# Optimization experiments

Measured on AMD Instinct MI355X. Metric: run time of the kernel, lower is better.

## Reference

```python
import jax, jax.numpy as jnp
import numpy as np

B, T, HOR = 4096, 128, 24
EH, DH, A = 64, 64, 32


def setup_inputs() -> dict:
    key = jax.random.key(0)
    ks = jax.random.split(key, 21)
    g = lambda k, shape, s=0.1: (jax.random.normal(k, shape, jnp.float32) * s)
    return {
        "x": jax.random.normal(ks[0], (B, T, 1), jnp.float32),
        # encoder GRUCell (input_size=1)
        "W_ih_e": g(ks[1], (3 * EH, 1)), "W_hh_e": g(ks[2], (3 * EH, EH)),
        "b_ih_e": g(ks[3], (3 * EH,)), "b_hh_e": g(ks[4], (3 * EH,)),
        # encoder input attention
        "W_e": g(ks[5], (A, EH)), "U_e": g(ks[6], (1, A)),
        "b_e": jnp.zeros((1, A), jnp.float32), "v_e": g(ks[7], (A,)),
        # decoder init
        "W_init": g(ks[8], (DH, EH)), "b_init": g(ks[9], (DH,)),
        # decoder GRUCell (input_size=1)
        "W_ih_d": g(ks[10], (3 * DH, 1)), "W_hh_d": g(ks[11], (3 * DH, DH)),
        "b_ih_d": g(ks[12], (3 * DH,)), "b_hh_d": g(ks[13], (3 * DH,)),
        # temporal attention
        "W_d": g(ks[14], (A, DH)), "U_d": g(ks[15], (A, EH)), "v_d": g(ks[16], (A,)),
        # output head
        "W_out": g(ks[17], (1, DH + EH)), "b_out": g(ks[18], (1,)),
        "y0": jnp.zeros((1,), jnp.float32),
    }


def _gru_cell(x, h, W_ih, W_hh, b_ih, b_hh):
    # PyTorch GRUCell semantics
    gi = x @ W_ih.T + b_ih  # (B, 3H)
    gh = h @ W_hh.T + b_hh
    ir, iz, inn = jnp.split(gi, 3, axis=1)
    hr, hz, hn = jnp.split(gh, 3, axis=1)
    r = jax.nn.sigmoid(ir + hr)
    z = jax.nn.sigmoid(iz + hz)
    n = jnp.tanh(inn + r * hn)
    return (1.0 - z) * n + z * h


def reference(x, W_ih_e, W_hh_e, b_ih_e, b_hh_e, W_e, U_e, b_e, v_e,
              W_init, b_init, W_ih_d, W_hh_d, b_ih_d, b_hh_d,
              W_d, U_d, v_d, W_out, b_out, y0):
    bsz = x.shape[0]

    def enc_step(h, x_t):  # x_t: (B, 1)
        h_proj = h @ W_e.T  # (B, A)
        attn = jnp.tanh(h_proj[:, None, :] + x_t[:, :, None] * U_e[None] + b_e[None])  # (B,1,A)
        scores = jnp.sum(attn * v_e, axis=2)  # (B, 1)
        alpha = jax.nn.softmax(scores, axis=1)
        h_new = _gru_cell(alpha * x_t, h, W_ih_e, W_hh_e, b_ih_e, b_hh_e)
        return h_new, h_new

    h0 = jnp.zeros((bsz, EH), x.dtype)
    h_T, Hs = jax.lax.scan(enc_step, h0, jnp.swapaxes(x, 0, 1))  # Hs: (T,B,EH)
    H = jnp.swapaxes(Hs, 0, 1)  # (B, T, EH)

    d0 = h_T @ W_init.T + b_init  # (B, DH)
    H_proj = jnp.einsum('bte,ae->bta', H, U_d)  # hoisted: constant across decoder steps
    dec_in0 = jnp.broadcast_to(y0[None, :], (bsz, 1))

    def dec_step(carry, _):
        d, dec_in = carry
        d = _gru_cell(dec_in, d, W_ih_d, W_hh_d, b_ih_d, b_hh_d)
        d_proj = d @ W_d.T  # (B, A)
        attn = jnp.tanh(d_proj[:, None, :] + H_proj)  # (B, T, A)
        beta = jax.nn.softmax(jnp.sum(attn * v_d, axis=2), axis=1)  # (B, T)
        ctx = jnp.einsum('bt,bte->be', beta, H)  # (B, EH)
        out = jnp.concatenate([d, ctx], axis=1) @ W_out.T + b_out  # (B, 1)
        return (d, out), out[:, 0]

    (_, _), outs = jax.lax.scan(dec_step, (d0, dec_in0), None, length=HOR)
    return outs.T  # (B, horizon)
```

## Files before the change

### kernel.cpp

```cpp
#include <hip/hip_runtime.h>
#include <math.h>

#define BATCH 4096
#define T 128
#define HOR 24

#define LOG2E 1.44269504088896f
#define C2    2.88539008177793f

typedef _Float16 half2_t __attribute__((ext_vector_type(2)));
typedef _Float16 half8   __attribute__((ext_vector_type(8)));
typedef float f2  __attribute__((ext_vector_type(2)));
typedef float f4v __attribute__((ext_vector_type(4)));

__device__ __forceinline__ float fexp2(float x){ return __builtin_amdgcn_exp2f(x); }
__device__ __forceinline__ float frcp(float x){ return __builtin_amdgcn_rcpf(x); }
__device__ __forceinline__ float fsig(float x){ return frcp(1.0f + fexp2(-LOG2E*x)); }
__device__ __forceinline__ float ftanh(float x){ return fmaf(-2.0f, frcp(1.0f + fexp2(C2*x)), 1.0f); }
__device__ __forceinline__ half2_t bch(unsigned u){ return __builtin_bit_cast(half2_t,u); }
__device__ __forceinline__ unsigned pk2(float a,float b){ return __builtin_bit_cast(unsigned, __builtin_amdgcn_cvt_pkrtz(a,b)); }
__device__ __forceinline__ unsigned pk2rne(float a,float b){
  half2_t h; h.x = (_Float16)a; h.y = (_Float16)b;
  return __builtin_bit_cast(unsigned, h);
}
__device__ __forceinline__ float fdot2f(half2_t a, half2_t b, float c){
#if __has_builtin(__builtin_amdgcn_fdot2)
  return __builtin_amdgcn_fdot2(a,b,c,false);
#else
  return fmaf((float)a.x,(float)b.x, fmaf((float)a.y,(float)b.y,c));
#endif
}
__device__ __forceinline__ f2 pkfma(f2 a, f2 b, f2 c){ return __builtin_elementwise_fma(a,b,c); }

template <int CTRL, int RMASK>
__device__ __forceinline__ float dpp_add(float v) {
  int s = __builtin_amdgcn_update_dpp(0, __builtin_bit_cast(int, v), CTRL, RMASK, 0xf, true);
  return v + __builtin_bit_cast(float, s);
}
__device__ __forceinline__ float wavesum_dpp(float v) {
  v = dpp_add<0x111, 0xf>(v);
  v = dpp_add<0x112, 0xf>(v);
  v = dpp_add<0x114, 0xf>(v);
  v = dpp_add<0x118, 0xf>(v);
  v = dpp_add<0x142, 0xa>(v);
  v = dpp_add<0x143, 0xc>(v);
  return v;
}
__device__ __forceinline__ float rdl63(float v){
  return __builtin_bit_cast(float, __builtin_amdgcn_readlane(__builtin_bit_cast(int, v), 63));
}

#define WG_BARRIER_LDS() do {                                   \
    asm volatile("s_waitcnt lgkmcnt(0)" ::: "memory");          \
    __builtin_amdgcn_s_barrier();                               \
  } while (0)

__device__ __forceinline__ void gru_mv(const _Float16* hrow,
    const unsigned* wr_r, const unsigned* wr_z, const unsigned* wr_n,
    float& ar0, float& ar1, float& az0, float& az1, float& an0, float& an1)
{
  const uint4* hq = (const uint4*)hrow;
  #pragma unroll
  for (int q = 0; q < 8; ++q) {
    uint4 hv = hq[q];
    ar0 = fdot2f(bch(hv.x), bch(wr_r[4*q+0]), ar0);
    az0 = fdot2f(bch(hv.x), bch(wr_z[4*q+0]), az0);
    an0 = fdot2f(bch(hv.x), bch(wr_n[4*q+0]), an0);
    ar1 = fdot2f(bch(hv.y), bch(wr_r[4*q+1]), ar1);
    az1 = fdot2f(bch(hv.y), bch(wr_z[4*q+1]), az1);
    an1 = fdot2f(bch(hv.y), bch(wr_n[4*q+1]), an1);
    ar0 = fdot2f(bch(hv.z), bch(wr_r[4*q+2]), ar0);
    az0 = fdot2f(bch(hv.z), bch(wr_z[4*q+2]), az0);
    an0 = fdot2f(bch(hv.z), bch(wr_n[4*q+2]), an0);
    ar1 = fdot2f(bch(hv.w), bch(wr_r[4*q+3]), ar1);
    az1 = fdot2f(bch(hv.w), bch(wr_z[4*q+3]), az1);
    an1 = fdot2f(bch(hv.w), bch(wr_n[4*q+3]), an1);
  }
}

__device__ __forceinline__ float proj_dot(const _Float16* base, const unsigned* udr)
{
  float acc = 0.f;
  const uint4* hb = (const uint4*)base;
  #pragma unroll
  for (int q = 0; q < 4; ++q) {
    uint4 hv = hb[q];
    acc = fdot2f(bch(hv.x), bch(udr[4*q+0]), acc);
    acc = fdot2f(bch(hv.y), bch(udr[4*q+1]), acc);
    acc = fdot2f(bch(hv.z), bch(udr[4*q+2]), acc);
    acc = fdot2f(bch(hv.w), bch(udr[4*q+3]), acc);
  }
  return acc;
}

__device__ __forceinline__ half8 cvt8(f4v a, f4v b){
  half8 h;
  h[0]=(_Float16)a.x; h[1]=(_Float16)a.y; h[2]=(_Float16)a.z; h[3]=(_Float16)a.w;
  h[4]=(_Float16)b.x; h[5]=(_Float16)b.y; h[6]=(_Float16)b.z; h[7]=(_Float16)b.w;
  return h;
}

__global__ __launch_bounds__(256, 1)
void darnn_enc(const float* __restrict__ x,
               const float* __restrict__ W_ih_e, const float* __restrict__ W_hh_e,
               const float* __restrict__ b_ih_e, const float* __restrict__ b_hh_e,
               const float* __restrict__ U_d, const float* __restrict__ W_out,
               unsigned* __restrict__ hpG, float* __restrict__ hTG)
{
  const int tid = threadIdx.x;
  const int w = tid >> 6;
  const int l = tid & 63;
  const int c = l & 15;
  const int q = l >> 4;
  const int e0 = blockIdx.x * 16;
  const int m0 = 16*w + 4*q;

  __shared__ __align__(16) _Float16 He[2][16*72];
  __shared__ __align__(16) unsigned xw[16*65];
  __shared__ __align__(16) unsigned ehC[2][16*273];

  for (int idx = tid; idx < 16*64; idx += 256) {
    int e = idx >> 6, j = idx & 63;
    f2 g = ((const f2*)(x + (size_t)(e0+e)*T))[j];
    xw[e*65 + j] = pk2(g.x, g.y);
  }
  for (int idx = tid; idx < 576; idx += 256) ((unsigned*)He[0])[idx] = 0;

  half8 Ar[2], Az[2], An[2];
  #pragma unroll
  for (int kap = 0; kap < 2; ++kap) {
    const f4v* pr = (const f4v*)(W_hh_e + (size_t)(16*w + c)*64       + 32*kap + 8*q);
    const f4v* pz = (const f4v*)(W_hh_e + (size_t)(64 + 16*w + c)*64  + 32*kap + 8*q);
    const f4v* pn = (const f4v*)(W_hh_e + (size_t)(128 + 16*w + c)*64 + 32*kap + 8*q);
    Ar[kap] = cvt8(pr[0], pr[1]);
    Az[kap] = cvt8(pz[0], pz[1]);
    An[kap] = cvt8(pn[0], pn[1]);
  }
  half8 AX[2] = {{0,0,0,0,0,0,0,0},{0,0,0,0,0,0,0,0}};
  if (w < 2) {
    #pragma unroll
    for (int kap = 0; kap < 2; ++kap) {
      const f4v* p = (const f4v*)(U_d + (size_t)(16*w + c)*64 + 32*kap + 8*q);
      AX[kap] = cvt8(p[0] * C2, p[1] * C2);
    }
  } else if (w == 2 && c == 0) {
    #pragma unroll
    for (int kap = 0; kap < 2; ++kap) {
      const f4v* p = (const f4v*)(W_out + 64 + 32*kap + 8*q);
      AX[kap] = cvt8(p[0], p[1]);
    }
  }
  f4v wih0 = *(const f4v*)(W_ih_e + m0);
  f4v wih1 = *(const f4v*)(W_ih_e + 64 + m0);
  f4v wih2 = *(const f4v*)(W_ih_e + 128 + m0);
  f4v bb0  = *(const f4v*)(b_ih_e + m0)      + *(const f4v*)(b_hh_e + m0);
  f4v bb1  = *(const f4v*)(b_ih_e + 64 + m0) + *(const f4v*)(b_hh_e + 64 + m0);
  f4v bi2  = *(const f4v*)(b_ih_e + 128 + m0);
  f4v bh2  = *(const f4v*)(b_hh_e + 128 + m0);
  f4v hreg = {0,0,0,0};
  const f4v z4 = {0,0,0,0};

  __syncthreads();

  #pragma unroll 1
  for (int t = 0; t < T; ++t) {
    if ((t & 15) == 1 && t > 16) {
      int cidx = (t - 17) >> 4;
      const unsigned* sbuf = ehC[cidx & 1];
      int t0 = cidx << 4;
      #pragma unroll
      for (int it = 0; it < 17; ++it) {
        int idx = tid + it*256;
        int e = idx / 272;
        int o = idx - e*272;
        hpG[(size_t)(e0+e)*2176 + t0*17 + o] = sbuf[e*273 + o];
      }
    }
    const _Float16* Hc = He[t & 1];
    half8 B0 = __builtin_bit_cast(half8, *(const uint4*)(Hc + c*72 + 8*q));
    half8 B1 = __builtin_bit_cast(half8, *(const uint4*)(Hc + c*72 + 32 + 8*q));
    if (t > 0) {
      unsigned* eb = ehC[((t-1) >> 4) & 1] + c*273 + ((t-1) & 15)*17;
      if (w < 2) {
        f4v cu = __builtin_amdgcn_mfma_f32_16x16x32_f16(AX[0], B0, z4, 0,0,0);
        cu     = __builtin_amdgcn_mfma_f32_16x16x32_f16(AX[1], B1, cu, 0,0,0);
        float x0 = fexp2(fminf(cu[0], 15.5f));
        float x1 = fexp2(fminf(cu[1], 15.5f));
        float x2 = fexp2(fminf(cu[2], 15.5f));
        float x3 = fexp2(fminf(cu[3], 15.5f));
        eb[8*w + 2*q]   = pk2rne(x0, x1);
        eb[8*w + 2*q+1] = pk2rne(x2, x3);
      } else if (w == 2) {
        f4v cw = __builtin_amdgcn_mfma_f32_16x16x32_f16(AX[0], B0, z4, 0,0,0);
        cw     = __builtin_amdgcn_mfma_f32_16x16x32_f16(AX[1], B1, cw, 0,0,0);
        if (q == 0) ((float*)eb)[16] = cw[0];
      }
    }
    f4v gr = __builtin_amdgcn_mfma_f32_16x16x32_f16(Ar[0], B0, z4, 0,0,0);
    gr     = __builtin_amdgcn_mfma_f32_16x16x32_f16(Ar[1], B1, gr, 0,0,0);
    f4v gz = __builtin_amdgcn_mfma_f32_16x16x32_f16(Az[0], B0, z4, 0,0,0);
    gz     = __builtin_amdgcn_mfma_f32_16x16x32_f16(Az[1], B1, gz, 0,0,0);
    f4v gn = __builtin_amdgcn_mfma_f32_16x16x32_f16(An[0], B0, z4, 0,0,0);
    gn     = __builtin_amdgcn_mfma_f32_16x16x32_f16(An[1], B1, gn, 0,0,0);
    float xc = (float)((const _Float16*)xw)[c*130 + t];
    f4v hn;
    #pragma unroll
    for (int i = 0; i < 4; ++i) {
      float r  = fsig(fmaf(xc, wih0[i], bb0[i]) + gr[i]);
      float zf = fsig(fmaf(xc, wih1[i], bb1[i]) + gz[i]);
      float n  = ftanh(fmaf(xc, wih2[i], bi2[i]) + r*(gn[i] + bh2[i]));
      float h  = fmaf(zf, hreg[i] - n, n);
      hreg[i] = h;
      hn[i] = h;
    }
    uint2 wv; wv.x = pk2(hn[0], hn[1]); wv.y = pk2(hn[2], hn[3]);
    *(uint2*)(He[(t+1)&1] + c*72 + m0) = wv;
    WG_BARRIER_LDS();
  }
  {
    const _Float16* Hc = He[0];
    half8 B0 = __builtin_bit_cast(half8, *(const uint4*)(Hc + c*72 + 8*q));
    half8 B1 = __builtin_bit_cast(half8, *(const uint4*)(Hc + c*72 + 32 + 8*q));
    unsigned* eb = ehC[1] + c*273 + 15*17;
    if (w < 2) {
      f4v cu = __builtin_amdgcn_mfma_f32_16x16x32_f16(AX[0], B0, z4, 0,0,0);
      cu     = __builtin_amdgcn_mfma_f32_16x16x32_f16(AX[1], B1, cu, 0,0,0);
      float x0 = fexp2(fminf(cu[0], 15.5f));
      float x1 = fexp2(fminf(cu[1], 15.5f));
      float x2 = fexp2(fminf(cu[2], 15.5f));
      float x3 = fexp2(fminf(cu[3], 15.5f));
      eb[8*w + 2*q]   = pk2rne(x0, x1);
      eb[8*w + 2*q+1] = pk2rne(x2, x3);
    } else if (w == 2) {
      f4v cw = __builtin_amdgcn_mfma_f32_16x16x32_f16(AX[0], B0, z4, 0,0,0);
      cw     = __builtin_amdgcn_mfma_f32_16x16x32_f16(AX[1], B1, cw, 0,0,0);
      if (q == 0) ((float*)eb)[16] = cw[0];
    }
  }
  WG_BARRIER_LDS();
  {
    const unsigned* sbuf = ehC[1];
    #pragma unroll
    for (int it = 0; it < 17; ++it) {
      int idx = tid + it*256;
      int e = idx / 272;
      int o = idx - e*272;
      hpG[(size_t)(e0+e)*2176 + 112*17 + o] = sbuf[e*273 + o];
    }
  }
  #pragma unroll
  for (int i = 0; i < 4; ++i)
    hTG[(size_t)(e0 + c)*64 + m0 + i] = hreg[i];
}

__global__ __launch_bounds__(128, 2)
void darnn_dec(const float* __restrict__ W_init, const float* __restrict__ b_init,
               const float* __restrict__ W_ih_d, const float* __restrict__ W_hh_d,
               const float* __restrict__ b_ih_d, const float* __restrict__ b_hh_d,
               const float* __restrict__ W_d, const float* __restrict__ v_d,
               const float* __restrict__ W_out, const float* __restrict__ b_out,
               const float* __restrict__ y0,
               const unsigned* __restrict__ hpG, const float* __restrict__ hTG,
               float* __restrict__ out)
{
  const int tid = threadIdx.x;
  const int wid = tid >> 6;
  const int l   = tid & 63;
  const int bA  = 4*blockIdx.x + 2*wid;
  const int bB  = bA + 1;
  const int a    = l & 31;
  const int half = l >> 5;

  __shared__ __align__(16) unsigned char smem[36928];
  unsigned char* wbp = smem + wid*18464;
  unsigned* hpA   = (unsigned*)wbp;
  unsigned* hpB   = (unsigned*)(wbp + 8704);
  _Float16* ringA = (_Float16*)(wbp + 17408);
  _Float16* ringB = (_Float16*)(wbp + 17536);
  float*    dpA   = (float*)(wbp + 17664);
  float*    dpB   = (float*)(wbp + 17792);
  float*    hTA   = (float*)(wbp + 17920);
  float*    hTB   = (float*)(wbp + 18176);

  {
    const uint4* sA = (const uint4*)(hpG + (size_t)bA * 2176);
    const uint4* sB = (const uint4*)(hpG + (size_t)bB * 2176);
    #pragma unroll
    for (int it = 0; it < 8; ++it) {
      ((uint4*)hpA)[it*64 + l] = sA[it*64 + l];
      ((uint4*)hpB)[it*64 + l] = sB[it*64 + l];
    }
    const unsigned* rA = hpG + (size_t)bA*2176 + 2048;
    const unsigned* rB = hpG + (size_t)bB*2176 + 2048;
    hpA[2048 + l] = rA[l];      hpA[2112 + l] = rA[64 + l];
    hpB[2048 + l] = rB[l];      hpB[2112 + l] = rB[64 + l];
  }
  hTA[l] = hTG[(size_t)bA*64 + l];
  hTB[l] = hTG[(size_t)bB*64 + l];

  unsigned wr_r[32], wr_z[32], wr_n[32];
  {
    const f4v* wp = (const f4v*)W_hh_d;
    #pragma unroll
    for (int k = 0; k < 16; ++k) {
      f4v vr = wp[l*16 + k];
      f4v vz = wp[(64 + l)*16 + k];
      f4v vn = wp[(128 + l)*16 + k];
      wr_r[2*k] = pk2(vr.x, vr.y); wr_r[2*k+1] = pk2(vr.z, vr.w);
      wr_z[2*k] = pk2(vz.x, vz.y); wr_z[2*k+1] = pk2(vz.z, vz.w);
      wr_n[2*k] = pk2(vn.x, vn.y); wr_n[2*k+1] = pk2(vn.z, vn.w);
    }
  }
  float wih0 = W_ih_d[l], wih1 = W_ih_d[64+l], wih2 = W_ih_d[128+l];
  float bb0  = b_ih_d[l] + b_hh_d[l];
  float bb1  = b_ih_d[64+l] + b_hh_d[64+l];
  float bih2 = b_ih_d[128+l], bhh2 = b_hh_d[128+l];
  unsigned udr[16];
  {
    const f2* up = (const f2*)(W_d + a*64 + half*32);
    #pragma unroll
    for (int k = 0; k < 16; ++k) { f2 f = up[k]; udr[k] = pk2(f.x, f.y); }
  }
  float dprevA, dprevB;
  {
    const f4v* wi = (const f4v*)(W_init + l*64);
    const f4v* ga = (const f4v*)hTA;
    const f4v* gb = (const f4v*)hTB;
    f2 aa0={0,0}, aa1={0,0}, ba0={0,0}, ba1={0,0};
    #pragma unroll
    for (int k = 0; k < 16; ++k) {
      f4v wv = wi[k];
      f4v va = ga[k], vb = gb[k];
      aa0 = pkfma(wv.xy, va.xy, aa0);
      aa1 = pkfma(wv.zw, va.zw, aa1);
      ba0 = pkfma(wv.xy, vb.xy, ba0);
      ba1 = pkfma(wv.zw, vb.zw, ba1);
    }
    float bi = b_init[l];
    dprevA = bi + (aa0.x + aa0.y) + (aa1.x + aa1.y);
    dprevB = bi + (ba0.x + ba0.y) + (ba1.x + ba1.y);
  }
  float wout1 = W_out[l];
  float hw0A = __builtin_bit_cast(float, hpA[l*17 + 16]);
  float hw1A = __builtin_bit_cast(float, hpA[(64 + l)*17 + 16]);
  float hw0B = __builtin_bit_cast(float, hpB[l*17 + 16]);
  float hw1B = __builtin_bit_cast(float, hpB[(64 + l)*17 + 16]);
  float oprevA = y0[0], oprevB = y0[0];
  float bo = b_out[0];
  float c1;
  {
    float sv = v_d[a];
    sv += __shfl_xor(sv, 16); sv += __shfl_xor(sv, 8);
    sv += __shfl_xor(sv, 4);  sv += __shfl_xor(sv, 2); sv += __shfl_xor(sv, 1);
    c1 = LOG2E * sv;
  }
  ringA[l] = (_Float16)dprevA;
  ringB[l] = (_Float16)dprevB;

  const unsigned* hprA0 = hpA + l*17;
  const unsigned* hprA1 = hpA + (64 + l)*17;
  const unsigned* hprB0 = hpB + l*17;
  const unsigned* hprB1 = hpB + (64 + l)*17;

  #pragma unroll 1
  for (int s = 0; s < HOR; ++s) {
    float ar0A=0,ar1A=0,az0A=0,az1A=0,an0A=0,an1A=0;
    float ar0B=0,ar1B=0,az0B=0,az1B=0,an0B=0,an1B=0;
    gru_mv(ringA, wr_r, wr_z, wr_n, ar0A,ar1A,az0A,az1A,an0A,an1A);
    gru_mv(ringB, wr_r, wr_z, wr_n, ar0B,ar1B,az0B,az1B,an0B,an1B);
    float rA = fsig(fmaf(oprevA, wih0, bb0) + ar0A + ar1A);
    float zA = fsig(fmaf(oprevA, wih1, bb1) + az0A + az1A);
    float nA = ftanh(fmaf(oprevA, wih2, bih2) + rA * (an0A + an1A + bhh2));
    float dnewA = fmaf(zA, dprevA - nA, nA);
    float rB = fsig(fmaf(oprevB, wih0, bb0) + ar0B + ar1B);
    float zB = fsig(fmaf(oprevB, wih1, bb1) + az0B + az1B);
    float nB = ftanh(fmaf(oprevB, wih2, bih2) + rB * (an0B + an1B + bhh2));
    float dnewB = fmaf(zB, dprevB - nB, nB);
    dprevA = dnewA; dprevB = dnewB;
    ringA[l] = (_Float16)dnewA;
    ringB[l] = (_Float16)dnewB;
    {
      float accA = proj_dot(ringA + half*32, udr);
      float accB = proj_dot(ringB + half*32, udr);
      accA += __shfl_xor(accA, 32);
      accB += __shfl_xor(accB, 32);
      if (l < 32) {
        dpA[l] = fexp2(C2 * accA);
        dpB[l] = fexp2(C2 * accB);
      }
    }
    float rs0A = 0.f, rs1A = 0.f, rs0B = 0.f, rs1B = 0.f;
    #pragma unroll
    for (int j2 = 0; j2 < 8; ++j2) {
      f4v edA = *(const f4v*)&dpA[4*j2];
      f4v edB = *(const f4v*)&dpB[4*j2];
      half2_t haA0 = bch(hprA0[2*j2]), hbA0 = bch(hprA0[2*j2+1]);
      half2_t haA1 = bch(hprA1[2*j2]), hbA1 = bch(hprA1[2*j2+1]);
      half2_t haB0 = bch(hprB0[2*j2]), hbB0 = bch(hprB0[2*j2+1]);
      half2_t haB1 = bch(hprB1[2*j2]), hbB1 = bch(hprB1[2*j2+1]);
      float v0 = v_d[4*j2], v1 = v_d[4*j2+1], v2 = v_d[4*j2+2], v3 = v_d[4*j2+3];
      rs0A = fmaf(v0, frcp(fmaf(edA.x, (float)haA0.x, 1.0f)), rs0A);
      rs0B = fmaf(v0, frcp(fmaf(edB.x, (float)haB0.x, 1.0f)), rs0B);
      rs0A = fmaf(v1, frcp(fmaf(edA.y, (float)haA0.y, 1.0f)), rs0A);
      rs0B = fmaf(v1, frcp(fmaf(edB.y, (float)haB0.y, 1.0f)), rs0B);
      rs0A = fmaf(v2, frcp(fmaf(edA.z, (float)hbA0.x, 1.0f)), rs0A);
      rs0B = fmaf(v2, frcp(fmaf(edB.z, (float)hbB0.x, 1.0f)), rs0B);
      rs0A = fmaf(v3, frcp(fmaf(edA.w, (float)hbA0.y, 1.0f)), rs0A);
      rs0B = fmaf(v3, frcp(fmaf(edB.w, (float)hbB0.y, 1.0f)), rs0B);
      rs1A = fmaf(v0, frcp(fmaf(edA.x, (float)haA1.x, 1.0f)), rs1A);
      rs1B = fmaf(v0, frcp(fmaf(edB.x, (float)haB1.x, 1.0f)), rs1B);
      rs1A = fmaf(v1, frcp(fmaf(edA.y, (float)haA1.y, 1.0f)), rs1A);
      rs1B = fmaf(v1, frcp(fmaf(edB.y, (float)haB1.y, 1.0f)), rs1B);
      rs1A = fmaf(v2, frcp(fmaf(edA.z, (float)hbA1.x, 1.0f)), rs1A);
      rs1B = fmaf(v2, frcp(fmaf(edB.z, (float)hbB1.x, 1.0f)), rs1B);
      rs1A = fmaf(v3, frcp(fmaf(edA.w, (float)hbA1.y, 1.0f)), rs1A);
      rs1B = fmaf(v3, frcp(fmaf(edB.w, (float)hbB1.y, 1.0f)), rs1B);
    }
    float e0A = fexp2(fmaf(-C2, rs0A, c1));
    float e1A = fexp2(fmaf(-C2, rs1A, c1));
    float e0B = fexp2(fmaf(-C2, rs0B, c1));
    float e1B = fexp2(fmaf(-C2, rs1B, c1));
    float P0A = rdl63(wavesum_dpp(e0A + e1A));
    float P1A = rdl63(wavesum_dpp(fmaf(e0A, hw0A, e1A * hw1A)));
    float P2A = rdl63(wavesum_dpp(wout1 * dnewA));
    float P0B = rdl63(wavesum_dpp(e0B + e1B));
    float P1B = rdl63(wavesum_dpp(fmaf(e0B, hw0B, e1B * hw1B)));
    float P2B = rdl63(wavesum_dpp(wout1 * dnewB));
    float oA = fmaf(P1A, frcp(P0A), P2A + bo);
    float oB = fmaf(P1B, frcp(P0B), P2B + bo);
    if (l == 0) {
      out[(size_t)bA * HOR + s] = oA;
      out[(size_t)bB * HOR + s] = oB;
    }
    oprevA = oA; oprevB = oB;
  }
}

extern "C" void kernel_launch(void* const* d_in, const int* in_sizes, int n_in,
                              void* d_out, int out_size, void* d_ws, size_t ws_size,
                              hipStream_t stream) {
  const float* x      = (const float*)d_in[0];
  const float* W_ih_e = (const float*)d_in[1];
  const float* W_hh_e = (const float*)d_in[2];
  const float* b_ih_e = (const float*)d_in[3];
  const float* b_hh_e = (const float*)d_in[4];
  const float* W_init = (const float*)d_in[9];
  const float* b_init = (const float*)d_in[10];
  const float* W_ih_d = (const float*)d_in[11];
  const float* W_hh_d = (const float*)d_in[12];
  const float* b_ih_d = (const float*)d_in[13];
  const float* b_hh_d = (const float*)d_in[14];
  const float* W_d    = (const float*)d_in[15];
  const float* U_d    = (const float*)d_in[16];
  const float* v_d    = (const float*)d_in[17];
  const float* W_out  = (const float*)d_in[18];
  const float* b_out  = (const float*)d_in[19];
  const float* y0     = (const float*)d_in[20];
  float* outp = (float*)d_out;

  unsigned* hpG = (unsigned*)d_ws;
  float*    hTG = (float*)((char*)d_ws + (size_t)BATCH * 2176 * 4);

  darnn_enc<<<BATCH/16, 256, 0, stream>>>(x, W_ih_e, W_hh_e, b_ih_e, b_hh_e,
      U_d, W_out, hpG, hTG);
  darnn_dec<<<BATCH/4, 128, 0, stream>>>(W_init, b_init, W_ih_d, W_hh_d,
      b_ih_d, b_hh_d, W_d, v_d, W_out, b_out, y0, hpG, hTG, outp);
}
```

Measured before the change: 272.1 us.

## Write encoder projections directly to global and combine four reciprocals into one

The encoder stops staging its per-step exp-projection outputs in a shared-memory chunk buffer that is copied to global every 16 steps. Each wave now writes its values straight to global, which removes the periodic bulk copy and the final barrier but produces scattered narrow stores on every step. In the decoder attention loop, groups of four v/(1+e*h) terms are summed over a common denominator so only one reciprocal is needed per four terms, at the cost of extra multiplies. The decoder exponent is also clamped so the product of four denominators does not overflow.

```diff
diff --git a/kernel.cpp b/kernel.cpp
--- a/kernel.cpp
+++ b/kernel.cpp
@@ -100,6 +100,22 @@
   return h;
 }
 
+__device__ __forceinline__ float grp4(float acc, f4v ed,
+                                      half2_t ha, half2_t hb,
+                                      float v0, float v1, float v2, float v3)
+{
+  float a0 = fmaf(ed.x, (float)ha.x, 1.0f);
+  float a1 = fmaf(ed.y, (float)ha.y, 1.0f);
+  float a2 = fmaf(ed.z, (float)hb.x, 1.0f);
+  float a3 = fmaf(ed.w, (float)hb.y, 1.0f);
+  float d01 = a0 * a1;
+  float d23 = a2 * a3;
+  float n01 = fmaf(v0, a1, v1 * a0);
+  float n23 = fmaf(v2, a3, v3 * a2);
+  float nc  = fmaf(n01, d23, n23 * d01);
+  return fmaf(nc, frcp(d01 * d23), acc);
+}
+
 __global__ __launch_bounds__(256, 1)
 void darnn_enc(const float* __restrict__ x,
                const float* __restrict__ W_ih_e, const float* __restrict__ W_hh_e,
@@ -117,7 +133,6 @@
 
   __shared__ __align__(16) _Float16 He[2][16*72];
   __shared__ __align__(16) unsigned xw[16*65];
-  __shared__ __align__(16) unsigned ehC[2][16*273];
 
   for (int idx = tid; idx < 16*64; idx += 256) {
     int e = idx >> 6, j = idx & 63;
@@ -159,41 +174,30 @@
   f4v bh2  = *(const f4v*)(b_hh_e + 128 + m0);
   f4v hreg = {0,0,0,0};
   const f4v z4 = {0,0,0,0};
+  unsigned* hpB = hpG + (size_t)(e0 + c) * 2176;
 
   __syncthreads();
 
   #pragma unroll 1
   for (int t = 0; t < T; ++t) {
-    if ((t & 15) == 1 && t > 16) {
-      int cidx = (t - 17) >> 4;
-      const unsigned* sbuf = ehC[cidx & 1];
-      int t0 = cidx << 4;
-      #pragma unroll
-      for (int it = 0; it < 17; ++it) {
-        int idx = tid + it*256;
-        int e = idx / 272;
-        int o = idx - e*272;
-        hpG[(size_t)(e0+e)*2176 + t0*17 + o] = sbuf[e*273 + o];
-      }
-    }
     const _Float16* Hc = He[t & 1];
     half8 B0 = __builtin_bit_cast(half8, *(const uint4*)(Hc + c*72 + 8*q));
     half8 B1 = __builtin_bit_cast(half8, *(const uint4*)(Hc + c*72 + 32 + 8*q));
     if (t > 0) {
-      unsigned* eb = ehC[((t-1) >> 4) & 1] + c*273 + ((t-1) & 15)*17;
       if (w < 2) {
         f4v cu = __builtin_amdgcn_mfma_f32_16x16x32_f16(AX[0], B0, z4, 0,0,0);
         cu     = __builtin_amdgcn_mfma_f32_16x16x32_f16(AX[1], B1, cu, 0,0,0);
+        unsigned* hpE = hpB + (t-1)*17 + 8*w;
         float x0 = fexp2(fminf(cu[0], 15.5f));
         float x1 = fexp2(fminf(cu[1], 15.5f));
         float x2 = fexp2(fminf(cu[2], 15.5f));
         float x3 = fexp2(fminf(cu[3], 15.5f));
-        eb[8*w + 2*q]   = pk2rne(x0, x1);
-        eb[8*w + 2*q+1] = pk2rne(x2, x3);
+        hpE[2*q]   = pk2rne(x0, x1);
+        hpE[2*q+1] = pk2rne(x2, x3);
       } else if (w == 2) {
         f4v cw = __builtin_amdgcn_mfma_f32_16x16x32_f16(AX[0], B0, z4, 0,0,0);
         cw     = __builtin_amdgcn_mfma_f32_16x16x32_f16(AX[1], B1, cw, 0,0,0);
-        if (q == 0) ((float*)eb)[16] = cw[0];
+        if (q == 0) ((float*)(hpB + (t-1)*17))[16] = cw[0];
       }
     }
     f4v gr = __builtin_amdgcn_mfma_f32_16x16x32_f16(Ar[0], B0, z4, 0,0,0);
@@ -221,31 +225,20 @@
     const _Float16* Hc = He[0];
     half8 B0 = __builtin_bit_cast(half8, *(const uint4*)(Hc + c*72 + 8*q));
     half8 B1 = __builtin_bit_cast(half8, *(const uint4*)(Hc + c*72 + 32 + 8*q));
-    unsigned* eb = ehC[1] + c*273 + 15*17;
     if (w < 2) {
       f4v cu = __builtin_amdgcn_mfma_f32_16x16x32_f16(AX[0], B0, z4, 0,0,0);
       cu     = __builtin_amdgcn_mfma_f32_16x16x32_f16(AX[1], B1, cu, 0,0,0);
+      unsigned* hpE = hpB + 127*17 + 8*w;
       float x0 = fexp2(fminf(cu[0], 15.5f));
       float x1 = fexp2(fminf(cu[1], 15.5f));
       float x2 = fexp2(fminf(cu[2], 15.5f));
       float x3 = fexp2(fminf(cu[3], 15.5f));
-      eb[8*w + 2*q]   = pk2rne(x0, x1);
-      eb[8*w + 2*q+1] = pk2rne(x2, x3);
+      hpE[2*q]   = pk2rne(x0, x1);
+      hpE[2*q+1] = pk2rne(x2, x3);
     } else if (w == 2) {
       f4v cw = __builtin_amdgcn_mfma_f32_16x16x32_f16(AX[0], B0, z4, 0,0,0);
       cw     = __builtin_amdgcn_mfma_f32_16x16x32_f16(AX[1], B1, cw, 0,0,0);
-      if (q == 0) ((float*)eb)[16] = cw[0];
-    }
-  }
-  WG_BARRIER_LDS();
-  {
-    const unsigned* sbuf = ehC[1];
-    #pragma unroll
-    for (int it = 0; it < 17; ++it) {
-      int idx = tid + it*256;
-      int e = idx / 272;
-      int o = idx - e*272;
-      hpG[(size_t)(e0+e)*2176 + 112*17 + o] = sbuf[e*273 + o];
+      if (q == 0) ((float*)(hpB + 127*17))[16] = cw[0];
     }
   }
   #pragma unroll
@@ -385,8 +378,8 @@
       accA += __shfl_xor(accA, 32);
       accB += __shfl_xor(accB, 32);
       if (l < 32) {
-        dpA[l] = fexp2(C2 * accA);
-        dpB[l] = fexp2(C2 * accB);
+        dpA[l] = fexp2(fminf(C2 * accA, 15.5f));
+        dpB[l] = fexp2(fminf(C2 * accB, 15.5f));
       }
     }
     float rs0A = 0.f, rs1A = 0.f, rs0B = 0.f, rs1B = 0.f;
@@ -399,22 +392,10 @@
       half2_t haB0 = bch(hprB0[2*j2]), hbB0 = bch(hprB0[2*j2+1]);
       half2_t haB1 = bch(hprB1[2*j2]), hbB1 = bch(hprB1[2*j2+1]);
       float v0 = v_d[4*j2], v1 = v_d[4*j2+1], v2 = v_d[4*j2+2], v3 = v_d[4*j2+3];
-      rs0A = fmaf(v0, frcp(fmaf(edA.x, (float)haA0.x, 1.0f)), rs0A);
-      rs0B = fmaf(v0, frcp(fmaf(edB.x, (float)haB0.x, 1.0f)), rs0B);
-      rs0A = fmaf(v1, frcp(fmaf(edA.y, (float)haA0.y, 1.0f)), rs0A);
-      rs0B = fmaf(v1, frcp(fmaf(edB.y, (float)haB0.y, 1.0f)), rs0B);
-      rs0A = fmaf(v2, frcp(fmaf(edA.z, (float)hbA0.x, 1.0f)), rs0A);
-      rs0B = fmaf(v2, frcp(fmaf(edB.z, (float)hbB0.x, 1.0f)), rs0B);
-      rs0A = fmaf(v3, frcp(fmaf(edA.w, (float)hbA0.y, 1.0f)), rs0A);
-      rs0B = fmaf(v3, frcp(fmaf(edB.w, (float)hbB0.y, 1.0f)), rs0B);
-      rs1A = fmaf(v0, frcp(fmaf(edA.x, (float)haA1.x, 1.0f)), rs1A);
-      rs1B = fmaf(v0, frcp(fmaf(edB.x, (float)haB1.x, 1.0f)), rs1B);
-      rs1A = fmaf(v1, frcp(fmaf(edA.y, (float)haA1.y, 1.0f)), rs1A);
-      rs1B = fmaf(v1, frcp(fmaf(edB.y, (float)haB1.y, 1.0f)), rs1B);
-      rs1A = fmaf(v2, frcp(fmaf(edA.z, (float)hbA1.x, 1.0f)), rs1A);
-      rs1B = fmaf(v2, frcp(fmaf(edB.z, (float)hbB1.x, 1.0f)), rs1B);
-      rs1A = fmaf(v3, frcp(fmaf(edA.w, (float)hbA1.y, 1.0f)), rs1A);
-      rs1B = fmaf(v3, frcp(fmaf(edB.w, (float)hbB1.y, 1.0f)), rs1B);
+      rs0A = grp4(rs0A, edA, haA0, hbA0, v0, v1, v2, v3);
+      rs0B = grp4(rs0B, edB, haB0, hbB0, v0, v1, v2, v3);
+      rs1A = grp4(rs1A, edA, haA1, hbA1, v0, v1, v2, v3);
+      rs1B = grp4(rs1B, edB, haB1, hbB1, v0, v1, v2, v3);
     }
     float e0A = fexp2(fmaf(-C2, rs0A, c1));
     float e1A = fexp2(fmaf(-C2, rs1A, c1));
```

Result: faster. 264.2 us (-2.9%).
